# Optimization experiments

Hardware: AMD Instinct MI355X
Metric: run time of the kernel (lower is better)

Reference implementation:

```python
import jax, jax.numpy as jnp
import numpy as np

B, S, D = 4, 4096, 1024  # S = maxlength * 2, D = hidden_dim * 2 (bi-rnn)
MAXLENGTH = 2048
NEG_BIG = -2.0 ** 31


def setup_inputs() -> dict:
    key = jax.random.key(0)
    k1, k2, k3, k4, k5 = jax.random.split(key, 5)
    inputs = jax.random.normal(k1, (B, S, D), dtype=jnp.float32)
    length = jax.random.randint(k2, (B,), 1, MAXLENGTH + 1, dtype=jnp.int32)
    # torch code requires max(length)*2 == maxlength*2 for expand() to work
    length = length.at[0].set(MAXLENGTH)
    scale = 1.0 / np.sqrt(D)
    Wq = jax.random.normal(k3, (D, D), dtype=jnp.float32) * scale
    Wk = jax.random.normal(k4, (D, D), dtype=jnp.float32) * scale
    Wv = jax.random.normal(k5, (D, D), dtype=jnp.float32) * scale
    return {"inputs": inputs, "length": length, "Wq": Wq, "Wk": Wk,
            "Wv": Wv, "maxlength": MAXLENGTH}


def reference(inputs, length, Wq, Wk, Wv, maxlength):
    # nn.Linear (bias=False): y = x @ W.T
    Q = inputs @ Wq.T                      # [B, S, D]
    K = inputs @ Wk.T                      # [B, S, D]
    V = inputs @ Wv.T                      # [B, S, D]
    max_len = maxlength * 2
    sent_len = length.astype(jnp.float32) * 2.0      # [B]
    # key-padding mask, broadcast over query dim: [B, 1, max_len]
    mask = (jnp.arange(max_len, dtype=jnp.float32)[None, :] < sent_len[:, None])[:, None, :]
    alpha = jnp.einsum('bqd,bkd->bqk', Q, K)         # [B, S, S] (no 1/sqrt(d) scaling, as in source)
    alpha = jnp.where(mask, alpha, NEG_BIG)
    alpha = jax.nn.softmax(alpha, axis=2)
    out = jnp.einsum('bqk,bkd->bqd', alpha, V)       # [B, S, D]
    return out
```

## Files before the change

### kernel.cpp

```cpp
#include <hip/hip_runtime.h>


typedef __attribute__((ext_vector_type(4))) float floatx4;
typedef __attribute__((ext_vector_type(4))) int intx4;
typedef __attribute__((ext_vector_type(8))) short shortx8;
typedef unsigned short ushort_t;

__device__ __forceinline__ ushort_t f2bf(float f) {
  union { float f; unsigned u; } x; x.f = f;
  unsigned r = x.u + 0x7fffu + ((x.u >> 16) & 1u);
  return (ushort_t)(r >> 16);
}
__device__ __forceinline__ float bf2f(ushort_t h) {
  union { unsigned u; float f; } x; x.u = ((unsigned)h) << 16; return x.f;
}
__device__ __forceinline__ void quant8(float v, char& qh, char& ql) {
  float vs = v * 16.0f;
  float h = rintf(vs);
  h = fminf(fmaxf(h, -127.f), 127.f);
  float l = rintf((vs - h) * 256.0f);
  l = fminf(fmaxf(l, -127.f), 127.f);
  qh = (char)(int)h; ql = (char)(int)l;
}
__device__ __forceinline__ void quant8w(float v, char& qh, char& ql) {
  float vs = v * 512.0f;
  float h = rintf(vs);
  h = fminf(fmaxf(h, -127.f), 127.f);
  float l = rintf((vs - h) * 256.0f);
  l = fminf(fmaxf(l, -127.f), 127.f);
  qh = (char)(int)h; ql = (char)(int)l;
}

__device__ __forceinline__ void gload_lds16(const void* g, void* l) {
  __builtin_amdgcn_global_load_lds(
      (__attribute__((address_space(1))) void*)(uintptr_t)g,
      (__attribute__((address_space(3))) void*)(unsigned)(uintptr_t)l,
      16, 0, 0);
}

template<int N> __device__ __forceinline__ void wait_vm() {
  static_assert(N == 0 || N == 3 || N == 4 || N == 6 || N == 8 || N == 12,
                "bad vmcnt");
  if constexpr (N == 0)       asm volatile("s_waitcnt vmcnt(0)" ::: "memory");
  else if constexpr (N == 3)  asm volatile("s_waitcnt vmcnt(3)" ::: "memory");
  else if constexpr (N == 4)  asm volatile("s_waitcnt vmcnt(4)" ::: "memory");
  else if constexpr (N == 6)  asm volatile("s_waitcnt vmcnt(6)" ::: "memory");
  else if constexpr (N == 8)  asm volatile("s_waitcnt vmcnt(8)" ::: "memory");
  else if constexpr (N == 12) asm volatile("s_waitcnt vmcnt(12)" ::: "memory");
}
template<int NL> __device__ __forceinline__ void wait_chunk(int rem) {
  if (rem >= 2)      wait_vm<2 * NL>();
  else if (rem == 1) wait_vm<NL>();
  else               wait_vm<0>();
}
__device__ __forceinline__ void barrier_fenced() {
  asm volatile("" ::: "memory");
  __builtin_amdgcn_s_barrier();
  asm volatile("" ::: "memory");
}

template<int TM, int TN, int OMODE, int LMODE>
__global__ __launch_bounds__(256)
void gemm_bt(const ushort_t* __restrict__ A0g, const ushort_t* __restrict__ B0g,
             void* __restrict__ C0v, int K, int lda, int ldc, long bstride,
             const int* __restrict__ lenp, int b0, long sA, long sB, long sC)
{
  constexpr int BM = TM * 32, BN = TN * 32;
  constexpr int LA = TM / 2, LB = TN / 2;
  constexpr int NL = LA + LB;
  constexpr int BUFA = BM * 32, BUFB = BN * 32;
  __shared__ ushort_t As[3][BM][32];
  __shared__ ushort_t Bs[3][BN][32];

  const int tid = threadIdx.x;
  const int z = blockIdx.z;
  const long row0 = (long)blockIdx.x * BM;
  const long col0 = (long)blockIdx.y * BN;

  int kend = K;
  if constexpr (LMODE == 2) {
    const int sent = lenp[b0 + z] * 2;
    kend = (sent + 127) & ~127;
  } else if constexpr (LMODE == 3) {
    const int sent = lenp[row0 >> 12] * 2;
    if ((int)(row0 & 4095) >= ((sent + 127) & ~127)) return;
  }

  const int sr = tid >> 2, scol = (tid & 3) * 8;
  const ushort_t* pA = A0g + z * sA + (row0 + sr) * (long)lda + scol;
  const ushort_t* pB = B0g + z * sB + (col0 + sr) * (long)K + scol;
  ushort_t* lA = &As[0][sr][scol];
  ushort_t* lB = &Bs[0][sr][scol];
  const long jA = 64 * (long)lda, jB = 64 * (long)K;

  const int wid = tid >> 6, lane = tid & 63;
  const int wm = (wid >> 1) * (BM / 2), wn = (wid & 1) * (BN / 2);
  const int lr = lane & 15, lq = lane >> 4;

  floatx4 acc[TM][TN] = {};

  auto stage = [&](int buf, int k0) {
#pragma unroll
    for (int j = 0; j < LA; ++j)
      gload_lds16(pA + k0 + j * jA, lA + buf * BUFA + j * 2048);
#pragma unroll
    for (int j = 0; j < LB; ++j)
      gload_lds16(pB + k0 + j * jB, lB + buf * BUFB + j * 2048);
  };

  const int nk = kend >> 5;
  stage(0, 0);
  stage(1, 32);
  int cur = 0, nx2 = 2;
  for (int t = 0; t < nk; ++t) {
    if (t + 2 < nk) stage(nx2, (t + 2) << 5);
    wait_chunk<NL>(nk - 1 - t);
    barrier_fenced();

    const ushort_t* Ab = &As[cur][0][0];
    const ushort_t* Bb = &Bs[cur][0][0];
    shortx8 af[TM], bf[TN];
#pragma unroll
    for (int tt = 0; tt < TM; ++tt)
      af[tt] = *(const shortx8*)&Ab[(wm + tt * 16 + lr) * 32 + lq * 8];
#pragma unroll
    for (int tt = 0; tt < TN; ++tt)
      bf[tt] = *(const shortx8*)&Bb[(wn + tt * 16 + lr) * 32 + lq * 8];
#pragma unroll
    for (int mt = 0; mt < TM; ++mt)
#pragma unroll
      for (int nt = 0; nt < TN; ++nt)
        acc[mt][nt] = __builtin_amdgcn_mfma_f32_16x16x32_bf16(af[mt], bf[nt], acc[mt][nt], 0, 0, 0);

    barrier_fenced();
    cur = (cur == 2) ? 0 : cur + 1;
    nx2 = (nx2 == 2) ? 0 : nx2 + 1;
  }

#pragma unroll
  for (int mt = 0; mt < TM; ++mt) {
#pragma unroll
    for (int nt = 0; nt < TN; ++nt) {
      long col = col0 + wn + nt * 16 + lr;
      if constexpr (OMODE == 2) {
        long row = row0 + wm + mt * 16 + lq * 4;
        long bb = row >> 12, s = row & 4095;
        ushort4 pk;
        pk.x = f2bf(acc[mt][nt][0]); pk.y = f2bf(acc[mt][nt][1]);
        pk.z = f2bf(acc[mt][nt][2]); pk.w = f2bf(acc[mt][nt][3]);
        *(ushort4*)&((ushort_t*)C0v)[bb * bstride + col * ldc + s] = pk;
      } else {
#pragma unroll
        for (int r = 0; r < 4; ++r) {
          long row = row0 + wm + mt * 16 + lq * 4 + r;
          ((float*)C0v)[z * sC + row * ldc + col] = acc[mt][nt][r];
        }
      }
    }
  }
}

__global__ __launch_bounds__(256)
void proj_i8(const char* __restrict__ Ah, const char* __restrict__ Al,
             const char* __restrict__ Bh, const char* __restrict__ Bl,
             char* __restrict__ CQh, char* __restrict__ CQl,
             char* __restrict__ CKh, char* __restrict__ CKl,
             const int* __restrict__ lenp)
{
  __shared__ char As[2][2][128][64];
  __shared__ char Bs[2][2][64][64];
  const int tid = threadIdx.x;
  const long row0 = (long)blockIdx.x * 128;
  const long col0 = (long)blockIdx.y * 64;
  const bool isK = col0 >= 1024;
  if (isK) {
    const int sent = lenp[row0 >> 12] * 2;
    if ((int)(row0 & 4095) >= ((sent + 127) & ~127)) return;
  }

  const int sr = tid >> 2, sc16 = (tid & 3) * 16;
  const char* pA0 = Ah + (row0 + sr) * 1024 + sc16;
  const char* pA1 = Al + (row0 + sr) * 1024 + sc16;
  const char* pB0 = Bh + (col0 + sr) * 1024 + sc16;
  const char* pB1 = Bl + (col0 + sr) * 1024 + sc16;
  char* lA0 = &As[0][0][sr][sc16];
  char* lA1 = &As[0][1][sr][sc16];
  char* lB0 = &Bs[0][0][sr][sc16];
  char* lB1 = &Bs[0][1][sr][sc16];

  const int wid = tid >> 6, lane = tid & 63;
  const int wm = (wid >> 1) * 64, wn = (wid & 1) * 32;
  const int lr = lane & 15, lq = lane >> 4;

  intx4 acc1[4][2] = {};
  intx4 acc2[4][2] = {};
  intx4 acc3[4][2] = {};

  auto stage = [&](int buf, int k0) {
#pragma unroll
    for (int j = 0; j < 2; ++j) {
      gload_lds16(pA0 + k0 + j * 65536, lA0 + buf * 16384 + j * 4096);
      gload_lds16(pA1 + k0 + j * 65536, lA1 + buf * 16384 + j * 4096);
    }
    gload_lds16(pB0 + k0, lB0 + buf * 8192);
    gload_lds16(pB1 + k0, lB1 + buf * 8192);
  };

  stage(0, 0);
  for (int t = 0; t < 16; ++t) {
    const int cur = t & 1;
    if (t + 1 < 16) { stage(cur ^ 1, (t + 1) << 6); wait_vm<6>(); }
    else           { wait_vm<0>(); }
    barrier_fenced();

    const char* Ab = &As[cur][0][0][0];
    const char* Bb = &Bs[cur][0][0][0];
    intx4 ah[4], al[4], bh[2], bl[2];
#pragma unroll
    for (int tt = 0; tt < 4; ++tt) {
      ah[tt] = *(const intx4*)&Ab[(wm + tt * 16 + lr) * 64 + lq * 16];
      al[tt] = *(const intx4*)&Ab[8192 + (wm + tt * 16 + lr) * 64 + lq * 16];
    }
#pragma unroll
    for (int tt = 0; tt < 2; ++tt) {
      bh[tt] = *(const intx4*)&Bb[(wn + tt * 16 + lr) * 64 + lq * 16];
      bl[tt] = *(const intx4*)&Bb[4096 + (wn + tt * 16 + lr) * 64 + lq * 16];
    }
#pragma unroll
    for (int mt = 0; mt < 4; ++mt)
#pragma unroll
      for (int nt = 0; nt < 2; ++nt) {
        acc1[mt][nt] = __builtin_amdgcn_mfma_i32_16x16x64_i8(ah[mt], bh[nt], acc1[mt][nt], 0, 0, 0);
        acc2[mt][nt] = __builtin_amdgcn_mfma_i32_16x16x64_i8(ah[mt], bl[nt], acc2[mt][nt], 0, 0, 0);
        acc2[mt][nt] = __builtin_amdgcn_mfma_i32_16x16x64_i8(al[mt], bh[nt], acc2[mt][nt], 0, 0, 0);
        acc3[mt][nt] = __builtin_amdgcn_mfma_i32_16x16x64_i8(al[mt], bl[nt], acc3[mt][nt], 0, 0, 0);
      }
    barrier_fenced();
  }

  char* __restrict__ Ch = isK ? CKh : CQh;
  char* __restrict__ Cl = isK ? CKl : CQl;
  const long cbase = col0 & 1023;
#pragma unroll
  for (int mt = 0; mt < 4; ++mt)
#pragma unroll
    for (int nt = 0; nt < 2; ++nt) {
      long col = cbase + wn + nt * 16 + lr;
#pragma unroll
      for (int r = 0; r < 4; ++r) {
        long row = row0 + wm + mt * 16 + lq * 4 + r;
        float v = ((float)acc1[mt][nt][r]
                   + (float)acc2[mt][nt][r] * (1.0f / 256.0f)
                   + (float)acc3[mt][nt][r] * (1.0f / 65536.0f)) * (1.0f / 8192.0f);
        char qh, ql;
        quant8(v, qh, ql);
        Ch[row * 1024 + col] = qh;
        Cl[row * 1024 + col] = ql;
      }
    }
}

__global__ __launch_bounds__(256)
void qk_i8(const char* __restrict__ Qh, const char* __restrict__ Ql,
           const char* __restrict__ Kh, const char* __restrict__ Kl,
           short* __restrict__ sc, const int* __restrict__ lenp, int b0)
{
  __shared__ char As[3][2][128][64];
  __shared__ char Bs[3][2][64][64];
  const int tid = threadIdx.x;
  const int z = blockIdx.z;
  const long zo = (long)z * 4096 * 1024;
  const long row0 = (long)blockIdx.x * 128;
  const long col0 = (long)blockIdx.y * 64;
  const int sent = lenp[b0 + z] * 2;
  if (col0 >= sent) return;

  const int sr = tid >> 2, sc16 = (tid & 3) * 16;
  const char* pA0 = Qh + zo + (row0 + sr) * 1024 + sc16;
  const char* pA1 = Ql + zo + (row0 + sr) * 1024 + sc16;
  const char* pB0 = Kh + zo + (col0 + sr) * 1024 + sc16;
  const char* pB1 = Kl + zo + (col0 + sr) * 1024 + sc16;
  char* lA0 = &As[0][0][sr][sc16];
  char* lA1 = &As[0][1][sr][sc16];
  char* lB0 = &Bs[0][0][sr][sc16];
  char* lB1 = &Bs[0][1][sr][sc16];

  const int wid = tid >> 6, lane = tid & 63;
  const int wm = (wid >> 1) * 64, wn = (wid & 1) * 32;
  const int lr = lane & 15, lq = lane >> 4;

  intx4 acc1[4][2] = {};
  intx4 acc2[4][2] = {};

  auto stage = [&](int buf, int k0) {
#pragma unroll
    for (int j = 0; j < 2; ++j) {
      gload_lds16(pA0 + k0 + j * 65536, lA0 + buf * 16384 + j * 4096);
      gload_lds16(pA1 + k0 + j * 65536, lA1 + buf * 16384 + j * 4096);
    }
    gload_lds16(pB0 + k0, lB0 + buf * 8192);
    gload_lds16(pB1 + k0, lB1 + buf * 8192);
  };

  stage(0, 0);
  stage(1, 64);
  int cur = 0, nx2 = 2;
  for (int t = 0; t < 16; ++t) {
    if (t + 2 < 16) stage(nx2, (t + 2) << 6);
    wait_chunk<6>(15 - t);
    barrier_fenced();

    const char* Ab = &As[cur][0][0][0];
    const char* Bb = &Bs[cur][0][0][0];
    intx4 ah[4], al[4], bh[2], bl[2];
#pragma unroll
    for (int tt = 0; tt < 4; ++tt) {
      ah[tt] = *(const intx4*)&Ab[(wm + tt * 16 + lr) * 64 + lq * 16];
      al[tt] = *(const intx4*)&Ab[8192 + (wm + tt * 16 + lr) * 64 + lq * 16];
    }
#pragma unroll
    for (int tt = 0; tt < 2; ++tt) {
      bh[tt] = *(const intx4*)&Bb[(wn + tt * 16 + lr) * 64 + lq * 16];
      bl[tt] = *(const intx4*)&Bb[4096 + (wn + tt * 16 + lr) * 64 + lq * 16];
    }
#pragma unroll
    for (int mt = 0; mt < 4; ++mt)
#pragma unroll
      for (int nt = 0; nt < 2; ++nt) {
        acc1[mt][nt] = __builtin_amdgcn_mfma_i32_16x16x64_i8(ah[mt], bh[nt], acc1[mt][nt], 0, 0, 0);
        acc2[mt][nt] = __builtin_amdgcn_mfma_i32_16x16x64_i8(ah[mt], bl[nt], acc2[mt][nt], 0, 0, 0);
        acc2[mt][nt] = __builtin_amdgcn_mfma_i32_16x16x64_i8(al[mt], bh[nt], acc2[mt][nt], 0, 0, 0);
      }
    barrier_fenced();
    cur = (cur == 2) ? 0 : cur + 1;
    nx2 = (nx2 == 2) ? 0 : nx2 + 1;
  }

  short* scz = sc + (long)z * 4096 * 4096;
#pragma unroll
  for (int mt = 0; mt < 4; ++mt)
#pragma unroll
    for (int nt = 0; nt < 2; ++nt) {
      long col = col0 + wn + nt * 16 + lr;
#pragma unroll
      for (int r = 0; r < 4; ++r) {
        long row = row0 + wm + mt * 16 + lq * 4 + r;
        float v = (float)acc1[mt][nt][r] * 0.125f
                + (float)acc2[mt][nt][r] * (1.0f / 2048.0f);
        v = fminf(fmaxf(v, -32000.0f), 32000.0f);
        scz[row * 4096 + col] = (short)(int)rintf(v);
      }
    }
}

__global__ __launch_bounds__(256)
void cast_split(const float* __restrict__ in, ushort_t* __restrict__ hi,
                char* __restrict__ qh, char* __restrict__ ql, int n4) {
  int i = blockIdx.x * 256 + threadIdx.x;
  if (i < n4) {
    float4 v = ((const float4*)in)[i];
    ushort4 h;
    h.x = f2bf(v.x); h.y = f2bf(v.y); h.z = f2bf(v.z); h.w = f2bf(v.w);
    ((ushort4*)hi)[i] = h;
    char ax, bx, ay, by, az, bz, aw, bw;
    quant8(v.x, ax, bx); quant8(v.y, ay, by);
    quant8(v.z, az, bz); quant8(v.w, aw, bw);
    char4 a, b;
    a.x = ax; a.y = ay; a.z = az; a.w = aw;
    b.x = bx; b.y = by; b.z = bz; b.w = bw;
    ((char4*)qh)[i] = a;
    ((char4*)ql)[i] = b;
  }
}

__global__ __launch_bounds__(256)
void cast_wqk(const float* __restrict__ w0, const float* __restrict__ w1,
              char* __restrict__ h0, char* __restrict__ l0,
              char* __restrict__ h1, char* __restrict__ l1, int n4) {
  int i = blockIdx.x * 256 + threadIdx.x;
  if (i >= n4) return;
  const float* in = blockIdx.y ? w1 : w0;
  char* hp = blockIdx.y ? h1 : h0;
  char* lp = blockIdx.y ? l1 : l0;
  float4 v = ((const float4*)in)[i];
  char ax, bx, ay, by, az, bz, aw, bw;
  quant8w(v.x, ax, bx); quant8w(v.y, ay, by);
  quant8w(v.z, az, bz); quant8w(v.w, aw, bw);
  char4 a, b;
  a.x = ax; a.y = ay; a.z = az; a.w = aw;
  b.x = bx; b.y = by; b.z = bz; b.w = bw;
  ((char4*)hp)[i] = a;
  ((char4*)lp)[i] = b;
}

__global__ __launch_bounds__(256)
void cast_wv(const float* __restrict__ w, ushort_t* __restrict__ h, int n4) {
  int i = blockIdx.x * 256 + threadIdx.x;
  if (i >= n4) return;
  float4 v = ((const float4*)w)[i];
  ushort4 p;
  p.x = f2bf(v.x); p.y = f2bf(v.y); p.z = f2bf(v.z); p.w = f2bf(v.w);
  ((ushort4*)h)[i] = p;
}

__global__ __launch_bounds__(256)
void softmax_rows(short* __restrict__ scores, const int* __restrict__ length, int b0) {
  const long row = blockIdx.x;
  const int b = b0 + (int)(row >> 12);
  short* p = scores + row * 4096;
  const int sent = length[b] * 2;
  const int sentceil = (sent + 127) & ~127;
  const int tid = threadIdx.x;
  float vals[16];
  float mx = -3.4e38f;
  int nj = 0;
  for (int c = tid; c < sentceil; c += 256) {
    float v = (float)p[c] * (1.0f / 32.0f);
    v = (c < sent) ? v : -2147483648.0f;
    vals[nj++] = v;
    mx = fmaxf(mx, v);
  }
#pragma unroll
  for (int off = 32; off > 0; off >>= 1) mx = fmaxf(mx, __shfl_down(mx, off));
  __shared__ float red[8];
  if ((tid & 63) == 0) red[tid >> 6] = mx;
  __syncthreads();
  mx = fmaxf(fmaxf(red[0], red[1]), fmaxf(red[2], red[3]));
  float sum = 0.f;
  for (int j = 0; j < nj; ++j) { vals[j] = __expf(vals[j] - mx); sum += vals[j]; }
#pragma unroll
  for (int off = 32; off > 0; off >>= 1) sum += __shfl_down(sum, off);
  __syncthreads();
  if ((tid & 63) == 0) red[tid >> 6] = sum;
  __syncthreads();
  float inv = 1.0f / (red[0] + red[1] + red[2] + red[3]);
  ushort_t* pb = (ushort_t*)p;
  int j = 0;
  for (int c = tid; c < sentceil; c += 256) pb[c] = f2bf(vals[j++] * inv);
}

extern "C" void kernel_launch(void* const* d_in, const int* in_sizes, int n_in,
                              void* d_out, int out_size, void* d_ws, size_t ws_size,
                              hipStream_t stream) {
  const float* X   = (const float*)d_in[0];
  const int*   len = (const int*)d_in[1];
  const float* Wq  = (const float*)d_in[2];
  const float* Wk  = (const float*)d_in[3];
  const float* Wv  = (const float*)d_in[4];
  float* out = (float*)d_out;

  const int Bn = 4, S = 4096, D = 1024;
  const long MS = (long)Bn * S;

  char* w = (char*)d_ws;
  ushort_t* Xhi = (ushort_t*)w; w += MS * D * 2;
  char* Xh8 = w; w += MS * D;
  char* Xl8 = w; w += MS * D;
  char* Qh8 = w; w += MS * D;
  char* Ql8 = w; w += MS * D;
  char* Kh8 = w; w += MS * D;
  char* Kl8 = w; w += MS * D;
  ushort_t* Vt  = (ushort_t*)w; w += MS * D * 2;
  char* WH8 = w; w += (long)2 * D * D;
  char* WL8 = w; w += (long)2 * D * D;
  ushort_t* Wvh = (ushort_t*)w; w += (long)D * D * 2;
  short* sc = (short*)d_ws;

  const int n4x = (int)(MS * D / 4);
  const int n4w = D * D / 4;
  cast_split<<<(n4x + 255) / 256, 256, 0, stream>>>(X, Xhi, Xh8, Xl8, n4x);
  cast_wqk<<<dim3((n4w + 255) / 256, 2), 256, 0, stream>>>(
      Wq, Wk, WH8, WL8, WH8 + (long)D * D, WL8 + (long)D * D, n4w);
  cast_wv<<<(n4w + 255) / 256, 256, 0, stream>>>(Wv, Wvh, n4w);

  dim3 blk(256);
  proj_i8<<<dim3(MS / 128, 2 * D / 64), blk, 0, stream>>>(
      Xh8, Xl8, WH8, WL8, Qh8, Ql8, Kh8, Kl8, len);
  gemm_bt<4, 4, 2, 3><<<dim3(MS / 128, D / 128, 1), blk, 0, stream>>>(
      Xhi, Wvh, Vt, D, D, S, (long)D * S, len, 0, 0, 0, 0);

  for (int p = 0; p < 2; ++p) {
    const int b0 = 2 * p;
    const long so = (long)b0 * S * D;
    qk_i8<<<dim3(S / 128, S / 64, 2), blk, 0, stream>>>(
        Qh8 + so, Ql8 + so, Kh8 + so, Kl8 + so, sc, len, b0);
    softmax_rows<<<2 * S, 256, 0, stream>>>(sc, len, b0);
    gemm_bt<4, 2, 0, 2><<<dim3(S / 128, D / 64, 2), blk, 0, stream>>>(
        (const ushort_t*)sc, Vt + (long)b0 * D * S, out + so, S, S, D, 0,
        len, b0, (long)S * 4096, (long)D * S, (long)S * D);
  }
}
```

Before: 617.9 us.

## Widen QK int8 tile to 128x128 with double buffering; split Q/K projection launches

The QK score kernel now computes 128x128 output tiles instead of 128x64, so each warp holds a 64x64 accumulator block. The staging ring drops from triple to double buffering with a simple wait-then-barrier scheme. The aim is more arithmetic per byte loaded from global memory and shared memory, at the cost of more accumulator registers, less pipelining depth, and coarser length-based skipping of padded key columns. The Q/K projection is also split into two templated launches so the runtime Q-versus-K branch becomes a compile-time choice.

```diff
diff --git a/kernel.cpp b/kernel.cpp
--- a/kernel.cpp
+++ b/kernel.cpp
@@ -160,11 +160,11 @@
   }
 }
 
+template<int LMODE>
 __global__ __launch_bounds__(256)
 void proj_i8(const char* __restrict__ Ah, const char* __restrict__ Al,
              const char* __restrict__ Bh, const char* __restrict__ Bl,
-             char* __restrict__ CQh, char* __restrict__ CQl,
-             char* __restrict__ CKh, char* __restrict__ CKl,
+             char* __restrict__ Ch, char* __restrict__ Cl,
              const int* __restrict__ lenp)
 {
   __shared__ char As[2][2][128][64];
@@ -172,8 +172,7 @@
   const int tid = threadIdx.x;
   const long row0 = (long)blockIdx.x * 128;
   const long col0 = (long)blockIdx.y * 64;
-  const bool isK = col0 >= 1024;
-  if (isK) {
+  if constexpr (LMODE == 3) {
     const int sent = lenp[row0 >> 12] * 2;
     if ((int)(row0 & 4095) >= ((sent + 127) & ~127)) return;
   }
@@ -238,14 +237,11 @@
     barrier_fenced();
   }
 
-  char* __restrict__ Ch = isK ? CKh : CQh;
-  char* __restrict__ Cl = isK ? CKl : CQl;
-  const long cbase = col0 & 1023;
 #pragma unroll
   for (int mt = 0; mt < 4; ++mt)
 #pragma unroll
     for (int nt = 0; nt < 2; ++nt) {
-      long col = cbase + wn + nt * 16 + lr;
+      long col = col0 + wn + nt * 16 + lr;
 #pragma unroll
       for (int r = 0; r < 4; ++r) {
         long row = row0 + wm + mt * 16 + lq * 4 + r;
@@ -265,13 +261,13 @@
            const char* __restrict__ Kh, const char* __restrict__ Kl,
            short* __restrict__ sc, const int* __restrict__ lenp, int b0)
 {
-  __shared__ char As[3][2][128][64];
-  __shared__ char Bs[3][2][64][64];
+  __shared__ char As[2][2][128][64];
+  __shared__ char Bs[2][2][128][64];
   const int tid = threadIdx.x;
   const int z = blockIdx.z;
   const long zo = (long)z * 4096 * 1024;
   const long row0 = (long)blockIdx.x * 128;
-  const long col0 = (long)blockIdx.y * 64;
+  const long col0 = (long)blockIdx.y * 128;
   const int sent = lenp[b0 + z] * 2;
   if (col0 >= sent) return;
 
@@ -286,61 +282,55 @@
   char* lB1 = &Bs[0][1][sr][sc16];
 
   const int wid = tid >> 6, lane = tid & 63;
-  const int wm = (wid >> 1) * 64, wn = (wid & 1) * 32;
+  const int wm = (wid >> 1) * 64, wn = (wid & 1) * 64;
   const int lr = lane & 15, lq = lane >> 4;
 
-  intx4 acc1[4][2] = {};
-  intx4 acc2[4][2] = {};
+  intx4 acc1[4][4] = {};
+  intx4 acc2[4][4] = {};
 
   auto stage = [&](int buf, int k0) {
 #pragma unroll
     for (int j = 0; j < 2; ++j) {
       gload_lds16(pA0 + k0 + j * 65536, lA0 + buf * 16384 + j * 4096);
       gload_lds16(pA1 + k0 + j * 65536, lA1 + buf * 16384 + j * 4096);
-    }
-    gload_lds16(pB0 + k0, lB0 + buf * 8192);
-    gload_lds16(pB1 + k0, lB1 + buf * 8192);
+      gload_lds16(pB0 + k0 + j * 65536, lB0 + buf * 16384 + j * 4096);
+      gload_lds16(pB1 + k0 + j * 65536, lB1 + buf * 16384 + j * 4096);
+    }
   };
 
   stage(0, 0);
-  stage(1, 64);
-  int cur = 0, nx2 = 2;
   for (int t = 0; t < 16; ++t) {
-    if (t + 2 < 16) stage(nx2, (t + 2) << 6);
-    wait_chunk<6>(15 - t);
+    const int cur = t & 1;
+    if (t + 1 < 16) { stage(cur ^ 1, (t + 1) << 6); wait_vm<8>(); }
+    else           { wait_vm<0>(); }
     barrier_fenced();
 
     const char* Ab = &As[cur][0][0][0];
     const char* Bb = &Bs[cur][0][0][0];
-    intx4 ah[4], al[4], bh[2], bl[2];
+    intx4 ah[4], al[4], bh[4], bl[4];
 #pragma unroll
     for (int tt = 0; tt < 4; ++tt) {
       ah[tt] = *(const intx4*)&Ab[(wm + tt * 16 + lr) * 64 + lq * 16];
       al[tt] = *(const intx4*)&Ab[8192 + (wm + tt * 16 + lr) * 64 + lq * 16];
-    }
-#pragma unroll
-    for (int tt = 0; tt < 2; ++tt) {
       bh[tt] = *(const intx4*)&Bb[(wn + tt * 16 + lr) * 64 + lq * 16];
-      bl[tt] = *(const intx4*)&Bb[4096 + (wn + tt * 16 + lr) * 64 + lq * 16];
+      bl[tt] = *(const intx4*)&Bb[8192 + (wn + tt * 16 + lr) * 64 + lq * 16];
     }
 #pragma unroll
     for (int mt = 0; mt < 4; ++mt)
 #pragma unroll
-      for (int nt = 0; nt < 2; ++nt) {
+      for (int nt = 0; nt < 4; ++nt) {
         acc1[mt][nt] = __builtin_amdgcn_mfma_i32_16x16x64_i8(ah[mt], bh[nt], acc1[mt][nt], 0, 0, 0);
         acc2[mt][nt] = __builtin_amdgcn_mfma_i32_16x16x64_i8(ah[mt], bl[nt], acc2[mt][nt], 0, 0, 0);
         acc2[mt][nt] = __builtin_amdgcn_mfma_i32_16x16x64_i8(al[mt], bh[nt], acc2[mt][nt], 0, 0, 0);
       }
     barrier_fenced();
-    cur = (cur == 2) ? 0 : cur + 1;
-    nx2 = (nx2 == 2) ? 0 : nx2 + 1;
   }
 
   short* scz = sc + (long)z * 4096 * 4096;
 #pragma unroll
   for (int mt = 0; mt < 4; ++mt)
 #pragma unroll
-    for (int nt = 0; nt < 2; ++nt) {
+    for (int nt = 0; nt < 4; ++nt) {
       long col = col0 + wn + nt * 16 + lr;
 #pragma unroll
       for (int r = 0; r < 4; ++r) {
@@ -474,15 +464,17 @@
   cast_wv<<<(n4w + 255) / 256, 256, 0, stream>>>(Wv, Wvh, n4w);
 
   dim3 blk(256);
-  proj_i8<<<dim3(MS / 128, 2 * D / 64), blk, 0, stream>>>(
-      Xh8, Xl8, WH8, WL8, Qh8, Ql8, Kh8, Kl8, len);
+  proj_i8<0><<<dim3(MS / 128, D / 64), blk, 0, stream>>>(
+      Xh8, Xl8, WH8, WL8, Qh8, Ql8, len);
+  proj_i8<3><<<dim3(MS / 128, D / 64), blk, 0, stream>>>(
+      Xh8, Xl8, WH8 + (long)D * D, WL8 + (long)D * D, Kh8, Kl8, len);
   gemm_bt<4, 4, 2, 3><<<dim3(MS / 128, D / 128, 1), blk, 0, stream>>>(
       Xhi, Wvh, Vt, D, D, S, (long)D * S, len, 0, 0, 0, 0);
 
   for (int p = 0; p < 2; ++p) {
     const int b0 = 2 * p;
     const long so = (long)b0 * S * D;
-    qk_i8<<<dim3(S / 128, S / 64, 2), blk, 0, stream>>>(
+    qk_i8<<<dim3(S / 128, S / 128, 2), blk, 0, stream>>>(
         Qh8 + so, Ql8 + so, Kh8 + so, Kl8 + so, sc, len, b0);
     softmax_rows<<<2 * S, 256, 0, stream>>>(sc, len, b0);
     gemm_bt<4, 2, 0, 2><<<dim3(S / 128, D / 64, 2), blk, 0, stream>>>(
```

After: 615.1 us. Within noise of the previous version (-0.5%).
